# Kernel optimization log

Hardware: AMD Instinct MI355X
Metric: run time of the kernel (lower is better)

Reference implementation:

```python
import jax, jax.numpy as jnp
import numpy as np


def setup_inputs() -> dict:
    key = jax.random.key(0)
    ks = jax.random.split(key, 9)
    B, IN, OUT, E, H = 64, 1024, 1024, 8, 8
    return {
        "x": jax.random.normal(ks[0], (B, IN), jnp.float32),
        "weight": jax.random.normal(ks[1], (E, OUT, IN), jnp.float32),
        "align_conv": jax.random.normal(ks[2], (E, E), jnp.float32),
        "W_ih": jax.random.normal(ks[3], (H, 1), jnp.float32),
        "W_hh": jax.random.normal(ks[4], (H, H), jnp.float32),
        "b_ih": jax.random.normal(ks[5], (H,), jnp.float32),
        "b_hh": jax.random.normal(ks[6], (H,), jnp.float32),
        "W_att": jax.random.normal(ks[7], (E, H), jnp.float32),
        "b_att": jax.random.normal(ks[8], (E,), jnp.float32),
    }


def reference(x, weight, align_conv, W_ih, W_hh, b_ih, b_hh, W_att, b_att):
    # attention_up: AdaptiveAvgPool1d(1) over feature dim -> [B, 1]
    pooled = jnp.mean(x, axis=-1, keepdims=True)  # [B, 1]
    # single-step tanh RNN, h0 = 0 (so W_hh contributes 0 in forward)
    h0 = jnp.zeros((x.shape[0], W_hh.shape[0]), x.dtype)
    h = jnp.tanh(pooled @ W_ih.T + h0 @ W_hh.T + b_ih + b_hh)  # [B, 8]
    # attention_down: ReLU -> Linear(8, E) -> Softmax over experts
    att = jax.nn.softmax(jax.nn.relu(h) @ W_att.T + b_att, axis=-1)  # [B, E]
    # align 1x1 conv over the expert axis: [E,E] x [E,out,in] -> [E,out,in]
    w_aligned = jnp.einsum('fe,eoi->foi', align_conv, weight)
    # per-sample fused weight [B, out, in] (the large intermediate)
    fuse_weight = jnp.einsum('be,eoi->boi', att, w_aligned)
    # per-sample matmul: [B,in] x [B,out,in] -> [B,out]
    y = jnp.einsum('bi,boi->bo', x, fuse_weight)
    return y
```

## Files before the change

### kernel.cpp

```cpp
#include <hip/hip_runtime.h>
#include <hip/hip_bf16.h>


typedef short bf16x8 __attribute__((ext_vector_type(8)));
typedef float f32x4 __attribute__((ext_vector_type(4)));

__device__ __forceinline__ unsigned short f2bf(float f) {
    unsigned int u = __builtin_bit_cast(unsigned int, f);
    u += 0x7fffu + ((u >> 16) & 1u);
    return (unsigned short)(u >> 16);
}

#define LDR 40

__global__ __launch_bounds__(64) void coef_kernel(
    const float* __restrict__ x,
    const float* __restrict__ align_conv,
    const float* __restrict__ W_ih,
    const float* __restrict__ b_ih,
    const float* __restrict__ b_hh,
    const float* __restrict__ W_att,
    const float* __restrict__ b_att,
    float* __restrict__ ct) {
    const int b = blockIdx.x;
    const int lane = threadIdx.x;
    const float4* x4 = (const float4*)x;
    float s = 0.f;
#pragma unroll
    for (int i = 0; i < 4; ++i) {
        float4 v = x4[b * 256 + lane + i * 64];
        s += v.x + v.y + v.z + v.w;
    }
#pragma unroll
    for (int off = 32; off > 0; off >>= 1) s += __shfl_down(s, off, 64);
    if (lane == 0) {
        float pooled = s * (1.0f / 1024.0f);
        float rl[8];
#pragma unroll
        for (int j = 0; j < 8; ++j) {
            float h = tanhf(pooled * W_ih[j] + b_ih[j] + b_hh[j]);
            rl[j] = h > 0.f ? h : 0.f;
        }
        float lg[8];
        float mx = -1e30f;
#pragma unroll
        for (int f = 0; f < 8; ++f) {
            float a = b_att[f];
#pragma unroll
            for (int j = 0; j < 8; ++j) a += rl[j] * W_att[f * 8 + j];
            lg[f] = a;
            mx = fmaxf(mx, a);
        }
        float den = 0.f;
#pragma unroll
        for (int f = 0; f < 8; ++f) { lg[f] = __expf(lg[f] - mx); den += lg[f]; }
        float inv = 1.0f / den;
#pragma unroll
        for (int e = 0; e < 8; ++e) {
            float c = 0.f;
#pragma unroll
            for (int f = 0; f < 8; ++f) c += lg[f] * inv * align_conv[f * 8 + e];
            ct[e * 64 + b] = c;
        }
    }
}

__global__ __launch_bounds__(256, 4) void zgemm_kernel(
    const float* __restrict__ x,
    const float* __restrict__ w,
    const float* __restrict__ ct,
    float* __restrict__ z) {
    __shared__ __align__(16) unsigned short xs[64 * LDR];
    __shared__ __align__(16) unsigned short wl[2][32 * LDR];
    __shared__ float csh[8 * 64];

    const int bid = blockIdx.x;
    const int ot = bid & 31;
    const int kc = bid >> 5;
    const int o0 = ot * 32;
    const int k0 = kc * 32;

    const int t = threadIdx.x;
    const int lane = t & 63;
    const int wid = t >> 6;
    const int quad = lane >> 4;
    const int lr = lane & 15;

    const float4* x4 = (const float4*)x;
    const float4* w4 = (const float4*)w;

#pragma unroll
    for (int it = 0; it < 2; ++it) {
        int f = t + it * 256, row = f >> 3, c4 = f & 7;
        float4 v = x4[row * 256 + (k0 >> 2) + c4];
        ushort4 p;
        p.x = f2bf(v.x); p.y = f2bf(v.y); p.z = f2bf(v.z); p.w = f2bf(v.w);
        *(ushort4*)&xs[row * LDR + c4 * 4] = p;
    }
    ((float2*)csh)[t] = ((const float2*)ct)[t];
    const int wrow = t >> 3, wc4 = t & 7;
    float4 wreg = w4[(o0 + wrow) * 256 + (k0 >> 2) + wc4];
    __syncthreads();

    bf16x8 bfrag = *(const bf16x8*)&xs[(wid * 16 + lr) * LDR + quad * 8];
    const int b = wid * 16 + lr;

    f32x4 accy[2];
    accy[0] = (f32x4){0.f, 0.f, 0.f, 0.f};
    accy[1] = (f32x4){0.f, 0.f, 0.f, 0.f};
    const f32x4 zero = (f32x4){0.f, 0.f, 0.f, 0.f};

    for (int e = 0; e < 8; ++e) {
        ushort4 p;
        p.x = f2bf(wreg.x); p.y = f2bf(wreg.y); p.z = f2bf(wreg.z); p.w = f2bf(wreg.w);
        *(ushort4*)&wl[e & 1][wrow * LDR + wc4 * 4] = p;
        __syncthreads();
        if (e < 7) wreg = w4[((e + 1) * 1024 + o0 + wrow) * 256 + (k0 >> 2) + wc4];
        float cv = csh[e * 64 + b];
#pragma unroll
        for (int mt = 0; mt < 2; ++mt) {
            bf16x8 afrag = *(const bf16x8*)&wl[e & 1][(mt * 16 + lr) * LDR + quad * 8];
            f32x4 d = __builtin_amdgcn_mfma_f32_16x16x32_bf16(afrag, bfrag, zero, 0, 0, 0);
#pragma unroll
            for (int rr = 0; rr < 4; ++rr) accy[mt][rr] += cv * d[rr];
        }
    }

#pragma unroll
    for (int mt = 0; mt < 2; ++mt) {
        float4 out;
        out.x = accy[mt][0]; out.y = accy[mt][1]; out.z = accy[mt][2]; out.w = accy[mt][3];
        *(float4*)&z[(((size_t)(kc * 64 + b)) << 10) + o0 + mt * 16 + quad * 4] = out;
    }
}

__global__ __launch_bounds__(256) void combine_kernel(
    const float* __restrict__ z,
    float* __restrict__ y) {
    const int bid = blockIdx.x;
    const int b = bid >> 2;
    const int oq = bid & 3;
    const int o = oq * 256 + threadIdx.x;
    float acc = 0.f;
#pragma unroll
    for (int kc = 0; kc < 32; ++kc)
        acc += z[(((size_t)(kc * 64 + b)) << 10) + o];
    y[(b << 10) + o] = acc;
}

extern "C" void kernel_launch(void* const* d_in, const int* in_sizes, int n_in,
                              void* d_out, int out_size, void* d_ws, size_t ws_size,
                              hipStream_t stream) {
    const float* x          = (const float*)d_in[0];
    const float* weight     = (const float*)d_in[1];
    const float* align_conv = (const float*)d_in[2];
    const float* W_ih       = (const float*)d_in[3];
    const float* b_ih       = (const float*)d_in[5];
    const float* b_hh       = (const float*)d_in[6];
    const float* W_att      = (const float*)d_in[7];
    const float* b_att      = (const float*)d_in[8];
    float* y = (float*)d_out;

    float* ct = (float*)d_ws;
    float* z  = (float*)((char*)d_ws + 4096);

    coef_kernel<<<dim3(64), dim3(64), 0, stream>>>(x, align_conv, W_ih, b_ih,
                                                   b_hh, W_att, b_att, ct);
    zgemm_kernel<<<dim3(1024), dim3(256), 0, stream>>>(x, weight, ct, z);
    combine_kernel<<<dim3(256), dim3(256), 0, stream>>>(z, y);
}
```

Baseline: 98.76 us.

## Fuse split-K reduction into GEMM via last-block atomic counter, widen K chunk

Each GEMM block now covers a 64-wide K slice (two MFMA steps chained per expert), which halves the grid and the size of the z partial buffer. The separate combine kernel is removed: every block increments a per-output-tile counter after a threadfence, and the last block for that tile sums the 16 partials into y. The counters are zeroed in the coefficient kernel. This saves one launch and half the partial-sum traffic, at the cost of a serial reduction tail in the last block of each tile and a lower occupancy hint.

After: 153.1 us. 1.55x slower.

```diff
diff --git a/kernel.cpp b/kernel.cpp
--- a/kernel.cpp
+++ b/kernel.cpp
@@ -11,7 +11,8 @@
     return (unsigned short)(u >> 16);
 }
 
-#define LDR 40
+#define XLDR 72
+#define WLDR 40
 
 __global__ __launch_bounds__(64) void coef_kernel(
     const float* __restrict__ x,
@@ -21,9 +22,11 @@
     const float* __restrict__ b_hh,
     const float* __restrict__ W_att,
     const float* __restrict__ b_att,
-    float* __restrict__ ct) {
+    float* __restrict__ ct,
+    int* __restrict__ cnt) {
     const int b = blockIdx.x;
     const int lane = threadIdx.x;
+    if (b == 0 && lane < 32) cnt[lane] = 0;
     const float4* x4 = (const float4*)x;
     float s = 0.f;
 #pragma unroll
@@ -65,20 +68,22 @@
     }
 }
 
-__global__ __launch_bounds__(256, 4) void zgemm_kernel(
+__global__ __launch_bounds__(256, 2) void zgemm_kernel(
     const float* __restrict__ x,
     const float* __restrict__ w,
     const float* __restrict__ ct,
-    float* __restrict__ z) {
-    __shared__ __align__(16) unsigned short xs[64 * LDR];
-    __shared__ __align__(16) unsigned short wl[2][32 * LDR];
-    __shared__ float csh[8 * 64];
+    float* __restrict__ z,
+    int* __restrict__ cnt,
+    float* __restrict__ y) {
+    __shared__ __align__(16) unsigned short xs[64 * XLDR];
+    __shared__ __align__(16) unsigned short wl[2][32 * WLDR];
+    __shared__ float csh[512];
+    __shared__ int isLast;
 
     const int bid = blockIdx.x;
     const int ot = bid & 31;
     const int kc = bid >> 5;
     const int o0 = ot * 32;
-    const int k0 = kc * 32;
 
     const int t = threadIdx.x;
     const int lane = t & 63;
@@ -90,39 +95,55 @@
     const float4* w4 = (const float4*)w;
 
 #pragma unroll
-    for (int it = 0; it < 2; ++it) {
-        int f = t + it * 256, row = f >> 3, c4 = f & 7;
-        float4 v = x4[row * 256 + (k0 >> 2) + c4];
-        ushort4 p;
-        p.x = f2bf(v.x); p.y = f2bf(v.y); p.z = f2bf(v.z); p.w = f2bf(v.w);
-        *(ushort4*)&xs[row * LDR + c4 * 4] = p;
+    for (int p = 0; p < 4; ++p) {
+        int row = (t >> 4) + p * 16, c4 = t & 15;
+        float4 v = x4[row * 256 + kc * 16 + c4];
+        ushort4 px;
+        px.x = f2bf(v.x); px.y = f2bf(v.y); px.z = f2bf(v.z); px.w = f2bf(v.w);
+        *(ushort4*)&xs[row * XLDR + c4 * 4] = px;
     }
     ((float2*)csh)[t] = ((const float2*)ct)[t];
+
     const int wrow = t >> 3, wc4 = t & 7;
-    float4 wreg = w4[(o0 + wrow) * 256 + (k0 >> 2) + wc4];
+    float4 wreg = w4[(o0 + wrow) * 256 + kc * 16 + wc4];
     __syncthreads();
 
-    bf16x8 bfrag = *(const bf16x8*)&xs[(wid * 16 + lr) * LDR + quad * 8];
     const int b = wid * 16 + lr;
+    bf16x8 bf0 = *(const bf16x8*)&xs[b * XLDR + quad * 8];
+    bf16x8 bf1 = *(const bf16x8*)&xs[b * XLDR + 32 + quad * 8];
 
-    f32x4 accy[2];
+    f32x4 accy[2], d[2];
     accy[0] = (f32x4){0.f, 0.f, 0.f, 0.f};
     accy[1] = (f32x4){0.f, 0.f, 0.f, 0.f};
     const f32x4 zero = (f32x4){0.f, 0.f, 0.f, 0.f};
 
-    for (int e = 0; e < 8; ++e) {
-        ushort4 p;
-        p.x = f2bf(wreg.x); p.y = f2bf(wreg.y); p.z = f2bf(wreg.z); p.w = f2bf(wreg.w);
-        *(ushort4*)&wl[e & 1][wrow * LDR + wc4 * 4] = p;
+    for (int ci = 0; ci < 16; ++ci) {
+        ushort4 pw;
+        pw.x = f2bf(wreg.x); pw.y = f2bf(wreg.y); pw.z = f2bf(wreg.z); pw.w = f2bf(wreg.w);
+        *(ushort4*)&wl[ci & 1][wrow * WLDR + wc4 * 4] = pw;
         __syncthreads();
-        if (e < 7) wreg = w4[((e + 1) * 1024 + o0 + wrow) * 256 + (k0 >> 2) + wc4];
-        float cv = csh[e * 64 + b];
+        if (ci < 15) {
+            int cn = ci + 1;
+            wreg = w4[((cn >> 1) * 1024 + o0 + wrow) * 256 + kc * 16 + (cn & 1) * 8 + wc4];
+        }
+        bf16x8 bcur = (ci & 1) ? bf1 : bf0;
+        if ((ci & 1) == 0) {
 #pragma unroll
-        for (int mt = 0; mt < 2; ++mt) {
-            bf16x8 afrag = *(const bf16x8*)&wl[e & 1][(mt * 16 + lr) * LDR + quad * 8];
-            f32x4 d = __builtin_amdgcn_mfma_f32_16x16x32_bf16(afrag, bfrag, zero, 0, 0, 0);
+            for (int mt = 0; mt < 2; ++mt) {
+                bf16x8 a = *(const bf16x8*)&wl[ci & 1][(mt * 16 + lr) * WLDR + quad * 8];
+                d[mt] = __builtin_amdgcn_mfma_f32_16x16x32_bf16(a, bcur, zero, 0, 0, 0);
+            }
+        } else {
+            float cv = csh[(ci >> 1) * 64 + b];
 #pragma unroll
-            for (int rr = 0; rr < 4; ++rr) accy[mt][rr] += cv * d[rr];
+            for (int mt = 0; mt < 2; ++mt) {
+                bf16x8 a = *(const bf16x8*)&wl[ci & 1][(mt * 16 + lr) * WLDR + quad * 8];
+                d[mt] = __builtin_amdgcn_mfma_f32_16x16x32_bf16(a, bcur, d[mt], 0, 0, 0);
+                accy[mt][0] += cv * d[mt][0];
+                accy[mt][1] += cv * d[mt][1];
+                accy[mt][2] += cv * d[mt][2];
+                accy[mt][3] += cv * d[mt][3];
+            }
         }
     }
 
@@ -132,20 +153,24 @@
         out.x = accy[mt][0]; out.y = accy[mt][1]; out.z = accy[mt][2]; out.w = accy[mt][3];
         *(float4*)&z[(((size_t)(kc * 64 + b)) << 10) + o0 + mt * 16 + quad * 4] = out;
     }
-}
 
-__global__ __launch_bounds__(256) void combine_kernel(
-    const float* __restrict__ z,
-    float* __restrict__ y) {
-    const int bid = blockIdx.x;
-    const int b = bid >> 2;
-    const int oq = bid & 3;
-    const int o = oq * 256 + threadIdx.x;
-    float acc = 0.f;
+    __threadfence();
+    if (t == 0) isLast = (atomicAdd(&cnt[ot], 1) == 15);
+    __syncthreads();
+    if (isLast) {
+        __threadfence();
+        const int oo = o0 + (t & 31);
+        const int tb = t >> 5;
 #pragma unroll
-    for (int kc = 0; kc < 32; ++kc)
-        acc += z[(((size_t)(kc * 64 + b)) << 10) + o];
-    y[(b << 10) + o] = acc;
+        for (int bb = 0; bb < 8; ++bb) {
+            int br = tb * 8 + bb;
+            float acc = 0.f;
+#pragma unroll
+            for (int k2 = 0; k2 < 16; ++k2)
+                acc += z[(((size_t)(k2 * 64 + br)) << 10) + oo];
+            y[(br << 10) + oo] = acc;
+        }
+    }
 }
 
 extern "C" void kernel_launch(void* const* d_in, const int* in_sizes, int n_in,
@@ -162,10 +187,10 @@
     float* y = (float*)d_out;
 
     float* ct = (float*)d_ws;
+    int*   cn = (int*)((char*)d_ws + 2048);
     float* z  = (float*)((char*)d_ws + 4096);
 
     coef_kernel<<<dim3(64), dim3(64), 0, stream>>>(x, align_conv, W_ih, b_ih,
-                                                   b_hh, W_att, b_att, ct);
-    zgemm_kernel<<<dim3(1024), dim3(256), 0, stream>>>(x, weight, ct, z);
-    combine_kernel<<<dim3(256), dim3(256), 0, stream>>>(z, y);
+                                                   b_hh, W_att, b_att, ct, cn);
+    zgemm_kernel<<<dim3(512), dim3(256), 0, stream>>>(x, weight, ct, z, cn, y);
 }
```
